# Optimization experiments

Hardware: AMD Instinct MI355X
Metric: run time of the kernel (lower is better)

## Reference

```python
import jax, jax.numpy as jnp
import numpy as np

BS, N, H = 8, 2048, 512
NEG_INF = -1.0e9
LEAKY_SLOPE = 0.01  # torch nn.LeakyReLU default


def setup_inputs() -> dict:
    key = jax.random.key(0)
    ks = jax.random.split(key, 8)
    feats = jax.random.normal(ks[0], (BS, N, H), dtype=jnp.float32)
    # random 0/1 adjacency with self-loops so every row has >=1 neighbor
    adj = jax.random.randint(ks[1], (BS, N, N), 0, 2).astype(jnp.float32)
    adj = jnp.maximum(adj, jnp.eye(N, dtype=jnp.float32)[None])
    s = 1.0 / np.sqrt(H)
    return {
        "feats": feats,
        "adj_mat": adj,
        "fc_w": jax.random.normal(ks[2], (H, H), dtype=jnp.float32) * s,
        "fc_b": jax.random.normal(ks[3], (H,), dtype=jnp.float32) * s,
        "q_w": jax.random.normal(ks[4], (1, H), dtype=jnp.float32) * s,
        "q_b": jax.random.normal(ks[5], (1,), dtype=jnp.float32) * s,
        "k_w": jax.random.normal(ks[6], (1, H), dtype=jnp.float32) * s,
        "k_b": jax.random.normal(ks[7], (1,), dtype=jnp.float32) * s,
    }


def reference(feats, adj_mat, fc_w, fc_b, q_w, q_b, k_w, k_b):
    # feats: [bs, N, H]; torch Linear: x @ W.T + b
    feat_proj = jnp.einsum("bnh,oh->bno", feats, fc_w) + fc_b          # [bs, N, H]
    q = jnp.einsum("bnh,oh->bno", feat_proj, q_w) + q_b                # [bs, N, 1]
    k = jnp.einsum("bnh,oh->bno", feat_proj, k_w) + k_b                # [bs, N, 1]
    logits = q + jnp.swapaxes(k, 2, 1)                                 # [bs, N, N] broadcast add
    masked = logits + (1.0 - adj_mat) * NEG_INF
    masked = jnp.where(masked >= 0, masked, LEAKY_SLOPE * masked)      # LeakyReLU
    atten = jax.nn.softmax(masked, axis=-1)
    # dropout is identity in eval mode
    out = jnp.einsum("bnm,bmh->bnh", atten, feat_proj)
    return out + feats  # residual=True
```

## Files before the change

kernel.cpp:

```cpp
#include <hip/hip_runtime.h>
#include <hip/hip_bf16.h>
#include <cstdint>
#include <cstddef>

#define BSZ 8
#define NN 2048
#define HH 512
#define MROWS (BSZ * NN)
#define LOG2E 1.44269504088896f

typedef __attribute__((ext_vector_type(4))) float f32x4;
typedef __attribute__((ext_vector_type(8))) short short8;
typedef __attribute__((ext_vector_type(4))) unsigned short us4;
typedef __attribute__((ext_vector_type(4))) uint32_t u32x4;

#if __has_builtin(__builtin_amdgcn_exp2f)
#define EXP2(x) __builtin_amdgcn_exp2f(x)
#else
#define EXP2(x) __expf((x) * 0.69314718056f)
#endif

static __device__ __forceinline__ unsigned short f2bf(float f) {
    uint32_t u = __builtin_bit_cast(uint32_t, f);
    u += 0x7fffu + ((u >> 16) & 1u);
    return (unsigned short)(u >> 16);
}

static __device__ __forceinline__ void async16(const unsigned short* g, unsigned short* l) {
    __builtin_amdgcn_global_load_lds(
        (const __attribute__((address_space(1))) void*)g,
        (__attribute__((address_space(3))) void*)l, 16, 0, 0);
}

__global__ __launch_bounds__(256) void prep_kernel(
    const float* __restrict__ feats, const float* __restrict__ fc_w,
    unsigned short* __restrict__ feats_bf, unsigned short* __restrict__ fcw_bf) {
    const int bid = blockIdx.x;
    const int tid = threadIdx.x;
    if (bid < 2048) {
        const int base = bid * 1024 + tid;
#pragma unroll
        for (int j = 0; j < 4; ++j) {
            const int i = base + j * 256;
            f32x4 v = ((const f32x4*)feats)[i];
            us4 o;
#pragma unroll
            for (int c = 0; c < 4; ++c) o[c] = f2bf(v[c]);
            ((us4*)feats_bf)[i] = o;
        }
    } else {
        const int base = (bid - 2048) * 1024 + tid;
#pragma unroll
        for (int j = 0; j < 4; ++j) {
            const int i = base + j * 256;
            f32x4 v = ((const f32x4*)fc_w)[i];
            us4 o;
#pragma unroll
            for (int c = 0; c < 4; ++c) o[c] = f2bf(v[c]);
            ((us4*)fcw_bf)[i] = o;
        }
    }
}

__global__ __launch_bounds__(256) void k2_kernel(
    const unsigned short* __restrict__ A, const unsigned short* __restrict__ Bt,
    const float* __restrict__ fc_b, const float* __restrict__ q_w,
    const float* __restrict__ k_w, const float* __restrict__ adj,
    unsigned short* __restrict__ fpT, unsigned char* __restrict__ maskb,
    float* __restrict__ qpart, float* __restrict__ kpart) {
    __shared__ alignas(16) unsigned short As[2][64 * 32];
    __shared__ alignas(16) unsigned short Bs[2][128 * 32];
    __shared__ float qred[2][64], kred[2][64];
    const int bid = blockIdx.x;
    const int tid = threadIdx.x;
    const int wave = tid >> 6, lane = tid & 63;
    if (bid % 3 == 0) {
        const int g = bid / 3;
        const int wi = wave >> 1, wj = wave & 1;
        const int n0 = (g & 3) * 128;
        const int i0 = (g >> 2) * 64;
        const int K = HH;
        const int lrow = lane >> 2;
        const int lseg = (lane & 3) * 8;
        const int fro = (lane & 15) * 32 + (lane >> 4) * 8;
        f32x4 acc[2][4];
#pragma unroll
        for (int a = 0; a < 2; ++a)
#pragma unroll
            for (int c = 0; c < 4; ++c) acc[a][c] = (f32x4)(0.f);

        auto stage = [&](int buf, int k0) {
            const unsigned short* ga = A + (size_t)(i0 + wave * 16 + lrow) * K + k0 + lseg;
            async16(ga, &As[buf][(wave * 16) * 32]);
            const unsigned short* gb = Bt + (size_t)(n0 + wave * 32 + lrow) * K + k0 + lseg;
            async16(gb, &Bs[buf][(wave * 32) * 32]);
            async16(gb + (size_t)16 * K, &Bs[buf][(wave * 32 + 16) * 32]);
        };

        stage(0, 0);
        __syncthreads();

        for (int k0 = 0; k0 < K; k0 += 32) {
            const int p = (k0 >> 5) & 1;
            if (k0 + 32 < K) stage(p ^ 1, k0 + 32);
            short8 af[2], bf[4];
#pragma unroll
            for (int t = 0; t < 2; ++t) af[t] = *(const short8*)&As[p][(wi * 32 + t * 16) * 32 + fro];
#pragma unroll
            for (int t = 0; t < 4; ++t) bf[t] = *(const short8*)&Bs[p][(wj * 64 + t * 16) * 32 + fro];
#pragma unroll
            for (int it = 0; it < 2; ++it)
#pragma unroll
                for (int jt = 0; jt < 4; ++jt)
                    acc[it][jt] = __builtin_amdgcn_mfma_f32_16x16x32_bf16(af[it], bf[jt], acc[it][jt], 0, 0, 0);
            __syncthreads();
        }

        int colv[4]; float cbv[4], qwv[4], kwv[4];
#pragma unroll
        for (int jt = 0; jt < 4; ++jt) {
            colv[jt] = n0 + wj * 64 + jt * 16 + (lane & 15);
            cbv[jt] = fc_b[colv[jt]];
            qwv[jt] = q_w[colv[jt]];
            kwv[jt] = k_w[colv[jt]];
        }
        const int b = i0 >> 11;
        const int il = i0 & 2047;
#pragma unroll
        for (int jt = 0; jt < 4; ++jt) {
#pragma unroll
            for (int it = 0; it < 2; ++it) {
                const int rb = wi * 32 + it * 16 + ((lane >> 4) << 2);
                us4 o;
#pragma unroll
                for (int r = 0; r < 4; ++r) o[r] = f2bf(acc[it][jt][r] + cbv[jt]);
                *(us4*)(fpT + ((size_t)b * HH + colv[jt]) * NN + il + rb) = o;
            }
        }
#pragma unroll
        for (int it = 0; it < 2; ++it) {
#pragma unroll
            for (int r = 0; r < 4; ++r) {
                float pq = 0.f, pk = 0.f;
#pragma unroll
                for (int jt = 0; jt < 4; ++jt) {
                    float v = acc[it][jt][r] + cbv[jt];
                    pq += v * qwv[jt];
                    pk += v * kwv[jt];
                }
                for (int off = 1; off < 16; off <<= 1) {
                    pq += __shfl_xor(pq, off, 64);
                    pk += __shfl_xor(pk, off, 64);
                }
                if ((lane & 15) == 0) {
                    const int rr = wi * 32 + it * 16 + ((lane >> 4) << 2) + r;
                    qred[wj][rr] = pq;
                    kred[wj][rr] = pk;
                }
            }
        }
        __syncthreads();
        if (tid < 64) {
            const size_t o = (size_t)(n0 >> 7) * MROWS + i0 + tid;
            qpart[o] = qred[0][tid] + qred[1][tid];
            kpart[o] = kred[0][tid] + kred[1][tid];
        }
    } else {
        const int a = (bid / 3) * 2 + (bid % 3) - 1;
#pragma unroll
        for (int s = 0; s < 2; ++s) {
            const int row = a * 8 + s * 4 + wave;
            const float* ar = adj + (size_t)row * NN;
#pragma unroll
            for (int p = 0; p < 4; ++p) {
                f32x4 v0 = *(const f32x4*)&ar[p * 512 + lane * 8];
                f32x4 v1 = *(const f32x4*)&ar[p * 512 + lane * 8 + 4];
                float fb = v0[0] + 2.f * v0[1] + 4.f * v0[2] + 8.f * v0[3]
                         + 16.f * v1[0] + 32.f * v1[1] + 64.f * v1[2] + 128.f * v1[3];
                maskb[(size_t)row * 256 + p * 64 + lane] = (unsigned char)(unsigned int)fb;
            }
        }
    }
}

__global__ __launch_bounds__(256) void fused_pv_kernel(
    const unsigned short* __restrict__ fpT, const unsigned char* __restrict__ maskb,
    const float* __restrict__ qpart, const float* __restrict__ kpart,
    const float* __restrict__ q_b, const float* __restrict__ k_b,
    const float* __restrict__ feats, float* __restrict__ out) {
    __shared__ alignas(16) unsigned short As[3][64 * 32];
    __shared__ alignas(16) unsigned short Bs[3][256 * 32];
    __shared__ float kLDS[NN];
    __shared__ float qLDS[64];
    __shared__ float rzl[64];
    const int tid = threadIdx.x;
    const int wave = tid >> 6, lane = tid & 63;
    const int wi = wave >> 1, wj = wave & 1;
    const int bid = blockIdx.x;
    const int b = bid & 7;
    const int t6 = bid >> 3;
    const int i0 = (t6 >> 1) * 64;
    const int n0 = (t6 & 1) * 256;
    const size_t rowbase = (size_t)b * NN + i0;

    {
        const float kb = k_b[0], qb = q_b[0];
#pragma unroll
        for (int s = 0; s < 8; ++s) {
            const int j = s * 256 + tid;
            const size_t gj = (size_t)b * NN + j;
            kLDS[j] = (kpart[gj] + kpart[MROWS + gj] + kpart[2 * MROWS + gj]
                     + kpart[3 * MROWS + gj] + kb) * LOG2E;
        }
        if (tid < 64) {
            const size_t gi = rowbase + tid;
            qLDS[tid] = (qpart[gi] + qpart[MROWS + gi] + qpart[2 * MROWS + gi]
                       + qpart[3 * MROWS + gi] + qb) * LOG2E;
        }
    }
    __syncthreads();

    const int r0 = tid >> 2;
    const int c8 = (tid & 3) * 8;
    const float qi = qLDS[r0];

    const unsigned short* Bt = fpT + (size_t)b * HH * NN;
    const uint32_t* mk = (const uint32_t*)maskb;
    const size_t mrow = (rowbase + r0) * 64;
    const int lrow = lane >> 2, lseg = (lane & 3) * 8;
    const int fro = (lane & 15) * 32 + (lane >> 4) * 8;

    auto stageB = [&](int buf, int k0) {
        const int rbase = wave * 64;
        const unsigned short* gb = Bt + (size_t)(n0 + rbase + lrow) * NN + k0 + lseg;
        async16(gb, &Bs[buf][rbase * 32]);
        async16(gb + (size_t)16 * NN, &Bs[buf][(rbase + 16) * 32]);
        async16(gb + (size_t)32 * NN, &Bs[buf][(rbase + 32) * 32]);
        async16(gb + (size_t)48 * NN, &Bs[buf][(rbase + 48) * 32]);
    };
    auto transform = [&](int buf, int k0, uint32_t mbits) {
        const f32x4 kv0 = *(const f32x4*)&kLDS[k0 + c8];
        const f32x4 kv1 = *(const f32x4*)&kLDS[k0 + c8 + 4];
        const uint32_t byte8 = (mbits >> c8) & 0xffu;
        float wv[8];
#pragma unroll
        for (int c = 0; c < 8; ++c) {
            float s = qi + (c < 4 ? kv0[c] : kv1[c - 4]);
            s = fmaxf(s, 0.01f * s);
            const float e = EXP2(s);
            wv[c] = ((byte8 >> c) & 1u) ? e : 0.f;
        }
        u32x4 pk;
#pragma unroll
        for (int p = 0; p < 4; ++p) {
            const uint32_t lo = __builtin_bit_cast(uint32_t, wv[2 * p]);
            const uint32_t hi = __builtin_bit_cast(uint32_t, wv[2 * p + 1]);
            pk[p] = __builtin_amdgcn_perm(hi, lo, 0x07060302u);
        }
        *(u32x4*)&As[buf][r0 * 32 + c8] = pk;
    };

    f32x4 acc[2][8];
#pragma unroll
    for (int a = 0; a < 2; ++a)
#pragma unroll
        for (int c = 0; c < 8; ++c) acc[a][c] = (f32x4)(0.f);
    f32x4 acc_z[2] = {(f32x4)(0.f), (f32x4)(0.f)};
    short8 ones;
#pragma unroll
    for (int j = 0; j < 8; ++j) ones[j] = (short)0x3F80;

    auto compute = [&](int rd) {
        short8 af[2], bf[8];
#pragma unroll
        for (int t = 0; t < 2; ++t) af[t] = *(const short8*)&As[rd][(wi * 32 + t * 16) * 32 + fro];
#pragma unroll
        for (int t = 0; t < 8; ++t) bf[t] = *(const short8*)&Bs[rd][(wj * 128 + t * 16) * 32 + fro];
        __builtin_amdgcn_s_setprio(1);
#pragma unroll
        for (int it = 0; it < 2; ++it)
#pragma unroll
            for (int jt = 0; jt < 8; ++jt)
                acc[it][jt] = __builtin_amdgcn_mfma_f32_16x16x32_bf16(af[it], bf[jt], acc[it][jt], 0, 0, 0);
        if (wj == 0) {
#pragma unroll
            for (int it = 0; it < 2; ++it)
                acc_z[it] = __builtin_amdgcn_mfma_f32_16x16x32_bf16(af[it], ones, acc_z[it], 0, 0, 0);
        }
        __builtin_amdgcn_s_setprio(0);
    };

    uint32_t mw_cur = mk[mrow];
    uint32_t mw_nxt = mk[mrow + 1];
    stageB(0, 0);
    transform(0, 0, mw_cur);
    asm volatile("s_waitcnt vmcnt(0)" ::: "memory");
    __builtin_amdgcn_sched_barrier(0);
    asm volatile("s_waitcnt lgkmcnt(0)" ::: "memory");
    __builtin_amdgcn_s_barrier();
    __builtin_amdgcn_sched_barrier(0);

    for (int j = 0; j < 62; ++j) {
        const int k0 = j * 32;
        const int rd = j % 3, st = (j + 1) % 3;
        uint32_t mnn;
        {
            const uint32_t* ma = mk + mrow + j + 2;
            asm volatile("global_load_dword %0, %1, off"
                         : "=v"(mnn) : "v"(ma) : "memory");
        }
        stageB(st, k0 + 32);
        asm volatile("s_waitcnt vmcnt(5)" ::: "memory");
        __builtin_amdgcn_sched_barrier(0);
        transform(st, k0 + 32, mw_nxt);
        mw_nxt = mnn;
        asm volatile("s_waitcnt lgkmcnt(0)" ::: "memory");
        __builtin_amdgcn_sched_barrier(0);
        __builtin_amdgcn_s_barrier();
        __builtin_amdgcn_sched_barrier(0);
        compute(rd);
    }
    {
        const int k0 = 62 * 32;
        stageB(0, k0 + 32);
        asm volatile("s_waitcnt vmcnt(4)" ::: "memory");
        __builtin_amdgcn_sched_barrier(0);
        transform(0, k0 + 32, mw_nxt);
        asm volatile("s_waitcnt lgkmcnt(0)" ::: "memory");
        __builtin_amdgcn_sched_barrier(0);
        __builtin_amdgcn_s_barrier();
        __builtin_amdgcn_sched_barrier(0);
        compute(62 % 3);
    }
    {
        asm volatile("s_waitcnt vmcnt(0)" ::: "memory");
        __builtin_amdgcn_sched_barrier(0);
        asm volatile("s_waitcnt lgkmcnt(0)" ::: "memory");
        __builtin_amdgcn_s_barrier();
        __builtin_amdgcn_sched_barrier(0);
        compute(0);
    }

    if (wj == 0 && (lane & 15) == 0) {
#pragma unroll
        for (int it = 0; it < 2; ++it) {
            const int rb = wi * 32 + it * 16 + ((lane >> 4) << 2);
#pragma unroll
            for (int r = 0; r < 4; ++r) rzl[rb + r] = 1.0f / acc_z[it][r];
        }
    }
    __syncthreads();

#pragma unroll
    for (int it = 0; it < 2; ++it) {
        const int rb = wi * 32 + it * 16 + ((lane >> 4) << 2);
        float rv[4];
#pragma unroll
        for (int r = 0; r < 4; ++r) rv[r] = rzl[rb + r];
#pragma unroll
        for (int jt = 0; jt < 8; ++jt) {
            const int col = n0 + wj * 128 + jt * 16 + (lane & 15);
#pragma unroll
            for (int r = 0; r < 4; ++r) {
                const size_t idx = (rowbase + rb + r) * HH + col;
                out[idx] = acc[it][jt][r] * rv[r] + feats[idx];
            }
        }
    }
}

extern "C" void kernel_launch(void* const* d_in, const int* in_sizes, int n_in,
                              void* d_out, int out_size, void* d_ws, size_t ws_size,
                              hipStream_t stream) {
    const float* feats = (const float*)d_in[0];
    const float* adj   = (const float*)d_in[1];
    const float* fc_w  = (const float*)d_in[2];
    const float* fc_b  = (const float*)d_in[3];
    const float* q_w   = (const float*)d_in[4];
    const float* q_b   = (const float*)d_in[5];
    const float* k_w   = (const float*)d_in[6];
    const float* k_b   = (const float*)d_in[7];
    float* out = (float*)d_out;

    char* w = (char*)d_ws;
    auto alloc = [&](size_t bytes) {
        char* p = w;
        w += (bytes + 255) & ~(size_t)255;
        return p;
    };
    unsigned short* feats_bf = (unsigned short*)alloc((size_t)BSZ * NN * HH * 2);
    unsigned short* fcw_bf   = (unsigned short*)alloc((size_t)HH * HH * 2);
    unsigned short* fpT   = (unsigned short*)alloc((size_t)BSZ * HH * NN * 2);
    unsigned char*  maskb = (unsigned char*)alloc((size_t)MROWS * 256);
    float* qpart = (float*)alloc((size_t)4 * MROWS * 4);
    float* kpart = (float*)alloc((size_t)4 * MROWS * 4);

    prep_kernel<<<2112, 256, 0, stream>>>(feats, fc_w, feats_bf, fcw_bf);
    k2_kernel<<<3072, 256, 0, stream>>>(feats_bf, fcw_bf, fc_b, q_w, k_w, adj,
                                        fpT, maskb, qpart, kpart);
    fused_pv_kernel<<<512, 256, 0, stream>>>(
        fpT, maskb, qpart, kpart, q_b, k_b, feats, out);
}
```

Before: 304.3 us.

## Fuse bf16 conversion into projection GEMM and retile PV warp layout

Removes the separate prep kernel that cast feats and fc_w to bf16. The projection GEMM now loads fp32 tiles into registers, converts them, and writes them to LDS, with register prefetch two steps ahead replacing async global-to-LDS copies. This saves a launch and a full round trip of the bf16 copy through memory, at the cost of more register pressure and conversion work inside the GEMM. Separately, the PV kernel changes its wave tiling from 2x2 (32 rows by 128 cols per wave) to 1x4 (all 64 rows by 64 cols per wave), and only wave 0 computes the row sums.

```diff
diff --git a/kernel.cpp b/kernel.cpp
--- a/kernel.cpp
+++ b/kernel.cpp
@@ -32,38 +32,8 @@
         (__attribute__((address_space(3))) void*)l, 16, 0, 0);
 }
 
-__global__ __launch_bounds__(256) void prep_kernel(
+__global__ __launch_bounds__(256) void k2_kernel(
     const float* __restrict__ feats, const float* __restrict__ fc_w,
-    unsigned short* __restrict__ feats_bf, unsigned short* __restrict__ fcw_bf) {
-    const int bid = blockIdx.x;
-    const int tid = threadIdx.x;
-    if (bid < 2048) {
-        const int base = bid * 1024 + tid;
-#pragma unroll
-        for (int j = 0; j < 4; ++j) {
-            const int i = base + j * 256;
-            f32x4 v = ((const f32x4*)feats)[i];
-            us4 o;
-#pragma unroll
-            for (int c = 0; c < 4; ++c) o[c] = f2bf(v[c]);
-            ((us4*)feats_bf)[i] = o;
-        }
-    } else {
-        const int base = (bid - 2048) * 1024 + tid;
-#pragma unroll
-        for (int j = 0; j < 4; ++j) {
-            const int i = base + j * 256;
-            f32x4 v = ((const f32x4*)fc_w)[i];
-            us4 o;
-#pragma unroll
-            for (int c = 0; c < 4; ++c) o[c] = f2bf(v[c]);
-            ((us4*)fcw_bf)[i] = o;
-        }
-    }
-}
-
-__global__ __launch_bounds__(256) void k2_kernel(
-    const unsigned short* __restrict__ A, const unsigned short* __restrict__ Bt,
     const float* __restrict__ fc_b, const float* __restrict__ q_w,
     const float* __restrict__ k_w, const float* __restrict__ adj,
     unsigned short* __restrict__ fpT, unsigned char* __restrict__ maskb,
@@ -79,41 +49,68 @@
         const int wi = wave >> 1, wj = wave & 1;
         const int n0 = (g & 3) * 128;
         const int i0 = (g >> 2) * 64;
-        const int K = HH;
-        const int lrow = lane >> 2;
-        const int lseg = (lane & 3) * 8;
         const int fro = (lane & 15) * 32 + (lane >> 4) * 8;
+        const int ar = tid & 63, ka = (tid >> 6) * 8;
+        const int br = tid & 127, kb = (tid >> 7) * 16;
         f32x4 acc[2][4];
 #pragma unroll
         for (int a = 0; a < 2; ++a)
 #pragma unroll
             for (int c = 0; c < 4; ++c) acc[a][c] = (f32x4)(0.f);
 
-        auto stage = [&](int buf, int k0) {
-            const unsigned short* ga = A + (size_t)(i0 + wave * 16 + lrow) * K + k0 + lseg;
-            async16(ga, &As[buf][(wave * 16) * 32]);
-            const unsigned short* gb = Bt + (size_t)(n0 + wave * 32 + lrow) * K + k0 + lseg;
-            async16(gb, &Bs[buf][(wave * 32) * 32]);
-            async16(gb + (size_t)16 * K, &Bs[buf][(wave * 32 + 16) * 32]);
+        f32x4 Ar[2][2], Br[2][4];
+        auto issue = [&](int s, int k0) {
+            const float* fa = feats + (size_t)(i0 + ar) * HH + k0 + ka;
+            Ar[s][0] = *(const f32x4*)fa;
+            Ar[s][1] = *(const f32x4*)(fa + 4);
+            const float* fb = fc_w + (size_t)(n0 + br) * HH + k0 + kb;
+#pragma unroll
+            for (int q = 0; q < 4; ++q) Br[s][q] = *(const f32x4*)(fb + q * 4);
         };
-
-        stage(0, 0);
-        __syncthreads();
-
-        for (int k0 = 0; k0 < K; k0 += 32) {
-            const int p = (k0 >> 5) & 1;
-            if (k0 + 32 < K) stage(p ^ 1, k0 + 32);
+        auto stw = [&](int s, int buf) {
+#pragma unroll
+            for (int h = 0; h < 2; ++h) {
+                us4 o;
+#pragma unroll
+                for (int c = 0; c < 4; ++c) o[c] = f2bf(Ar[s][h][c]);
+                *(us4*)&As[buf][ar * 32 + ka + h * 4] = o;
+            }
+#pragma unroll
+            for (int q = 0; q < 4; ++q) {
+                us4 o;
+#pragma unroll
+                for (int c = 0; c < 4; ++c) o[c] = f2bf(Br[s][q][c]);
+                *(us4*)&Bs[buf][br * 32 + kb + q * 4] = o;
+            }
+        };
+
+        issue(0, 0);
+        stw(0, 0);
+        issue(1, 32);
+        asm volatile("s_waitcnt lgkmcnt(0)" ::: "memory");
+        __builtin_amdgcn_s_barrier();
+        __builtin_amdgcn_sched_barrier(0);
+
+#pragma unroll
+        for (int j = 0; j < 16; ++j) {
+            const int p = j & 1;
             short8 af[2], bf[4];
 #pragma unroll
             for (int t = 0; t < 2; ++t) af[t] = *(const short8*)&As[p][(wi * 32 + t * 16) * 32 + fro];
 #pragma unroll
             for (int t = 0; t < 4; ++t) bf[t] = *(const short8*)&Bs[p][(wj * 64 + t * 16) * 32 + fro];
+            if (j < 14) issue(p, (j + 2) * 32);
+            if (j < 15) stw(p ^ 1, p ^ 1);
 #pragma unroll
             for (int it = 0; it < 2; ++it)
 #pragma unroll
                 for (int jt = 0; jt < 4; ++jt)
                     acc[it][jt] = __builtin_amdgcn_mfma_f32_16x16x32_bf16(af[it], bf[jt], acc[it][jt], 0, 0, 0);
-            __syncthreads();
+            if (j < 15) {
+                asm volatile("s_waitcnt lgkmcnt(0)" ::: "memory");
+                __builtin_amdgcn_s_barrier();
+                __builtin_amdgcn_sched_barrier(0);
+            }
         }
 
         int colv[4]; float cbv[4], qwv[4], kwv[4];
@@ -170,11 +167,11 @@
 #pragma unroll
         for (int s = 0; s < 2; ++s) {
             const int row = a * 8 + s * 4 + wave;
-            const float* ar = adj + (size_t)row * NN;
+            const float* ar2 = adj + (size_t)row * NN;
 #pragma unroll
             for (int p = 0; p < 4; ++p) {
-                f32x4 v0 = *(const f32x4*)&ar[p * 512 + lane * 8];
-                f32x4 v1 = *(const f32x4*)&ar[p * 512 + lane * 8 + 4];
+                f32x4 v0 = *(const f32x4*)&ar2[p * 512 + lane * 8];
+                f32x4 v1 = *(const f32x4*)&ar2[p * 512 + lane * 8 + 4];
                 float fb = v0[0] + 2.f * v0[1] + 4.f * v0[2] + 8.f * v0[3]
                          + 16.f * v1[0] + 32.f * v1[1] + 64.f * v1[2] + 128.f * v1[3];
                 maskb[(size_t)row * 256 + p * 64 + lane] = (unsigned char)(unsigned int)fb;
@@ -195,7 +192,6 @@
     __shared__ float rzl[64];
     const int tid = threadIdx.x;
     const int wave = tid >> 6, lane = tid & 63;
-    const int wi = wave >> 1, wj = wave & 1;
     const int bid = blockIdx.x;
     const int b = bid & 7;
     const int t6 = bid >> 3;
@@ -260,31 +256,31 @@
         *(u32x4*)&As[buf][r0 * 32 + c8] = pk;
     };
 
-    f32x4 acc[2][8];
-#pragma unroll
-    for (int a = 0; a < 2; ++a)
-#pragma unroll
-        for (int c = 0; c < 8; ++c) acc[a][c] = (f32x4)(0.f);
-    f32x4 acc_z[2] = {(f32x4)(0.f), (f32x4)(0.f)};
+    f32x4 acc[4][4];
+#pragma unroll
+    for (int a = 0; a < 4; ++a)
+#pragma unroll
+        for (int c = 0; c < 4; ++c) acc[a][c] = (f32x4)(0.f);
+    f32x4 acc_z[4] = {(f32x4)(0.f), (f32x4)(0.f), (f32x4)(0.f), (f32x4)(0.f)};
     short8 ones;
 #pragma unroll
     for (int j = 0; j < 8; ++j) ones[j] = (short)0x3F80;
 
     auto compute = [&](int rd) {
-        short8 af[2], bf[8];
-#pragma unroll
-        for (int t = 0; t < 2; ++t) af[t] = *(const short8*)&As[rd][(wi * 32 + t * 16) * 32 + fro];
-#pragma unroll
-        for (int t = 0; t < 8; ++t) bf[t] = *(const short8*)&Bs[rd][(wj * 128 + t * 16) * 32 + fro];
+        short8 af[4], bf[4];
+#pragma unroll
+        for (int t = 0; t < 4; ++t) af[t] = *(const short8*)&As[rd][(t * 16) * 32 + fro];
+#pragma unroll
+        for (int t = 0; t < 4; ++t) bf[t] = *(const short8*)&Bs[rd][(wave * 64 + t * 16) * 32 + fro];
         __builtin_amdgcn_s_setprio(1);
 #pragma unroll
-        for (int it = 0; it < 2; ++it)
-#pragma unroll
-            for (int jt = 0; jt < 8; ++jt)
+        for (int it = 0; it < 4; ++it)
+#pragma unroll
+            for (int jt = 0; jt < 4; ++jt)
                 acc[it][jt] = __builtin_amdgcn_mfma_f32_16x16x32_bf16(af[it], bf[jt], acc[it][jt], 0, 0, 0);
-        if (wj == 0) {
-#pragma unroll
-            for (int it = 0; it < 2; ++it)
+        if (wave == 0) {
+#pragma unroll
+            for (int it = 0; it < 4; ++it)
                 acc_z[it] = __builtin_amdgcn_mfma_f32_16x16x32_bf16(af[it], ones, acc_z[it], 0, 0, 0);
         }
         __builtin_amdgcn_s_setprio(0);
@@ -341,10 +337,10 @@
         compute(0);
     }
 
-    if (wj == 0 && (lane & 15) == 0) {
-#pragma unroll
-        for (int it = 0; it < 2; ++it) {
-            const int rb = wi * 32 + it * 16 + ((lane >> 4) << 2);
+    if (wave == 0 && (lane & 15) == 0) {
+#pragma unroll
+        for (int it = 0; it < 4; ++it) {
+            const int rb = it * 16 + ((lane >> 4) << 2);
 #pragma unroll
             for (int r = 0; r < 4; ++r) rzl[rb + r] = 1.0f / acc_z[it][r];
         }
@@ -352,14 +348,14 @@
     __syncthreads();
 
 #pragma unroll
-    for (int it = 0; it < 2; ++it) {
-        const int rb = wi * 32 + it * 16 + ((lane >> 4) << 2);
+    for (int it = 0; it < 4; ++it) {
+        const int rb = it * 16 + ((lane >> 4) << 2);
         float rv[4];
 #pragma unroll
         for (int r = 0; r < 4; ++r) rv[r] = rzl[rb + r];
 #pragma unroll
-        for (int jt = 0; jt < 8; ++jt) {
-            const int col = n0 + wj * 128 + jt * 16 + (lane & 15);
+        for (int jt = 0; jt < 4; ++jt) {
+            const int col = n0 + wave * 64 + jt * 16 + (lane & 15);
 #pragma unroll
             for (int r = 0; r < 4; ++r) {
                 const size_t idx = (rowbase + rb + r) * HH + col;
@@ -388,15 +384,12 @@
         w += (bytes + 255) & ~(size_t)255;
         return p;
     };
-    unsigned short* feats_bf = (unsigned short*)alloc((size_t)BSZ * NN * HH * 2);
-    unsigned short* fcw_bf   = (unsigned short*)alloc((size_t)HH * HH * 2);
     unsigned short* fpT   = (unsigned short*)alloc((size_t)BSZ * HH * NN * 2);
     unsigned char*  maskb = (unsigned char*)alloc((size_t)MROWS * 256);
     float* qpart = (float*)alloc((size_t)4 * MROWS * 4);
     float* kpart = (float*)alloc((size_t)4 * MROWS * 4);
 
-    prep_kernel<<<2112, 256, 0, stream>>>(feats, fc_w, feats_bf, fcw_bf);
-    k2_kernel<<<3072, 256, 0, stream>>>(feats_bf, fcw_bf, fc_b, q_w, k_w, adj,
+    k2_kernel<<<3072, 256, 0, stream>>>(feats, fc_w, fc_b, q_w, k_w, adj,
                                         fpT, maskb, qpart, kpart);
     fused_pv_kernel<<<512, 256, 0, stream>>>(
         fpT, maskb, qpart, kpart, q_b, k_b, feats, out);
```

Measured after the change: 338.4 us. +11.2%, slower.

## Triple-buffer projection GEMM and remap PV waves to 1x4 column split

Applied to the files above, without the earlier changes.

The projection GEMM in k2_kernel moves from double to triple-buffered LDS staging, with explicit vmcnt waits, a single barrier per step and raised MFMA priority, so global loads overlap compute further. In the fused PV kernel the 2x2 wave tiling becomes a 1x4 split: each wave covers all 64 rows and 64 columns, loading 4 A and 4 B fragments instead of 2 and 8. The row-sum MFMA now runs only on wave 0 but covers 4 row tiles. This trades more LDS use and a different balance of LDS fragment reads for better load overlap.

```diff
diff --git a/kernel.cpp b/kernel.cpp
--- a/kernel.cpp
+++ b/kernel.cpp
@@ -68,8 +68,8 @@
     const float* __restrict__ k_w, const float* __restrict__ adj,
     unsigned short* __restrict__ fpT, unsigned char* __restrict__ maskb,
     float* __restrict__ qpart, float* __restrict__ kpart) {
-    __shared__ alignas(16) unsigned short As[2][64 * 32];
-    __shared__ alignas(16) unsigned short Bs[2][128 * 32];
+    __shared__ alignas(16) unsigned short As[3][64 * 32];
+    __shared__ alignas(16) unsigned short Bs[3][128 * 32];
     __shared__ float qred[2][64], kred[2][64];
     const int bid = blockIdx.x;
     const int tid = threadIdx.x;
@@ -98,22 +98,34 @@
         };
 
         stage(0, 0);
-        __syncthreads();
-
-        for (int k0 = 0; k0 < K; k0 += 32) {
-            const int p = (k0 >> 5) & 1;
-            if (k0 + 32 < K) stage(p ^ 1, k0 + 32);
+        asm volatile("s_waitcnt vmcnt(0)" ::: "memory");
+        __builtin_amdgcn_sched_barrier(0);
+        __builtin_amdgcn_s_barrier();
+        __builtin_amdgcn_sched_barrier(0);
+
+        for (int j = 0; j < 16; ++j) {
+            if (j < 15) {
+                stage((j + 1) % 3, (j + 1) * 32);
+                asm volatile("s_waitcnt vmcnt(3)" ::: "memory");
+            } else {
+                asm volatile("s_waitcnt vmcnt(0)" ::: "memory");
+            }
+            __builtin_amdgcn_sched_barrier(0);
+            __builtin_amdgcn_s_barrier();
+            __builtin_amdgcn_sched_barrier(0);
+            const int p = j % 3;
             short8 af[2], bf[4];
 #pragma unroll
             for (int t = 0; t < 2; ++t) af[t] = *(const short8*)&As[p][(wi * 32 + t * 16) * 32 + fro];
 #pragma unroll
             for (int t = 0; t < 4; ++t) bf[t] = *(const short8*)&Bs[p][(wj * 64 + t * 16) * 32 + fro];
+            __builtin_amdgcn_s_setprio(1);
 #pragma unroll
             for (int it = 0; it < 2; ++it)
 #pragma unroll
                 for (int jt = 0; jt < 4; ++jt)
                     acc[it][jt] = __builtin_amdgcn_mfma_f32_16x16x32_bf16(af[it], bf[jt], acc[it][jt], 0, 0, 0);
-            __syncthreads();
+            __builtin_amdgcn_s_setprio(0);
         }
 
         int colv[4]; float cbv[4], qwv[4], kwv[4];
@@ -170,11 +182,11 @@
 #pragma unroll
         for (int s = 0; s < 2; ++s) {
             const int row = a * 8 + s * 4 + wave;
-            const float* ar = adj + (size_t)row * NN;
+            const float* ar2 = adj + (size_t)row * NN;
 #pragma unroll
             for (int p = 0; p < 4; ++p) {
-                f32x4 v0 = *(const f32x4*)&ar[p * 512 + lane * 8];
-                f32x4 v1 = *(const f32x4*)&ar[p * 512 + lane * 8 + 4];
+                f32x4 v0 = *(const f32x4*)&ar2[p * 512 + lane * 8];
+                f32x4 v1 = *(const f32x4*)&ar2[p * 512 + lane * 8 + 4];
                 float fb = v0[0] + 2.f * v0[1] + 4.f * v0[2] + 8.f * v0[3]
                          + 16.f * v1[0] + 32.f * v1[1] + 64.f * v1[2] + 128.f * v1[3];
                 maskb[(size_t)row * 256 + p * 64 + lane] = (unsigned char)(unsigned int)fb;
@@ -195,7 +207,6 @@
     __shared__ float rzl[64];
     const int tid = threadIdx.x;
     const int wave = tid >> 6, lane = tid & 63;
-    const int wi = wave >> 1, wj = wave & 1;
     const int bid = blockIdx.x;
     const int b = bid & 7;
     const int t6 = bid >> 3;
@@ -260,31 +271,31 @@
         *(u32x4*)&As[buf][r0 * 32 + c8] = pk;
     };
 
-    f32x4 acc[2][8];
-#pragma unroll
-    for (int a = 0; a < 2; ++a)
-#pragma unroll
-        for (int c = 0; c < 8; ++c) acc[a][c] = (f32x4)(0.f);
-    f32x4 acc_z[2] = {(f32x4)(0.f), (f32x4)(0.f)};
+    f32x4 acc[4][4];
+#pragma unroll
+    for (int a = 0; a < 4; ++a)
+#pragma unroll
+        for (int c = 0; c < 4; ++c) acc[a][c] = (f32x4)(0.f);
+    f32x4 acc_z[4] = {(f32x4)(0.f), (f32x4)(0.f), (f32x4)(0.f), (f32x4)(0.f)};
     short8 ones;
 #pragma unroll
     for (int j = 0; j < 8; ++j) ones[j] = (short)0x3F80;
 
     auto compute = [&](int rd) {
-        short8 af[2], bf[8];
-#pragma unroll
-        for (int t = 0; t < 2; ++t) af[t] = *(const short8*)&As[rd][(wi * 32 + t * 16) * 32 + fro];
-#pragma unroll
-        for (int t = 0; t < 8; ++t) bf[t] = *(const short8*)&Bs[rd][(wj * 128 + t * 16) * 32 + fro];
+        short8 af[4], bf[4];
+#pragma unroll
+        for (int t = 0; t < 4; ++t) af[t] = *(const short8*)&As[rd][(t * 16) * 32 + fro];
+#pragma unroll
+        for (int t = 0; t < 4; ++t) bf[t] = *(const short8*)&Bs[rd][(wave * 64 + t * 16) * 32 + fro];
         __builtin_amdgcn_s_setprio(1);
 #pragma unroll
-        for (int it = 0; it < 2; ++it)
-#pragma unroll
-            for (int jt = 0; jt < 8; ++jt)
+        for (int it = 0; it < 4; ++it)
+#pragma unroll
+            for (int jt = 0; jt < 4; ++jt)
                 acc[it][jt] = __builtin_amdgcn_mfma_f32_16x16x32_bf16(af[it], bf[jt], acc[it][jt], 0, 0, 0);
-        if (wj == 0) {
-#pragma unroll
-            for (int it = 0; it < 2; ++it)
+        if (wave == 0) {
+#pragma unroll
+            for (int it = 0; it < 4; ++it)
                 acc_z[it] = __builtin_amdgcn_mfma_f32_16x16x32_bf16(af[it], ones, acc_z[it], 0, 0, 0);
         }
         __builtin_amdgcn_s_setprio(0);
@@ -341,10 +352,10 @@
         compute(0);
     }
 
-    if (wj == 0 && (lane & 15) == 0) {
-#pragma unroll
-        for (int it = 0; it < 2; ++it) {
-            const int rb = wi * 32 + it * 16 + ((lane >> 4) << 2);
+    if (wave == 0 && (lane & 15) == 0) {
+#pragma unroll
+        for (int it = 0; it < 4; ++it) {
+            const int rb = it * 16 + ((lane >> 4) << 2);
 #pragma unroll
             for (int r = 0; r < 4; ++r) rzl[rb + r] = 1.0f / acc_z[it][r];
         }
@@ -352,14 +363,14 @@
     __syncthreads();
 
 #pragma unroll
-    for (int it = 0; it < 2; ++it) {
-        const int rb = wi * 32 + it * 16 + ((lane >> 4) << 2);
+    for (int it = 0; it < 4; ++it) {
+        const int rb = it * 16 + ((lane >> 4) << 2);
         float rv[4];
 #pragma unroll
         for (int r = 0; r < 4; ++r) rv[r] = rzl[rb + r];
 #pragma unroll
-        for (int jt = 0; jt < 8; ++jt) {
-            const int col = n0 + wj * 128 + jt * 16 + (lane & 15);
+        for (int jt = 0; jt < 4; ++jt) {
+            const int col = n0 + wave * 64 + jt * 16 + (lane & 15);
 #pragma unroll
             for (int r = 0; r < 4; ++r) {
                 const size_t idx = (rowbase + rb + r) * HH + col;
```

After: 306.0 us. No clear change (+0.5%).
